# Kernel tuning notes

Measured on AMD Instinct MI355X. Metric: run time of the kernel, lower is better.

Reference implementation:

```python
import jax, jax.numpy as jnp
import numpy as np

D_MODEL, D_HID, N_EXPERTS, TOP_K = 1024, 4096, 8, 2

def setup_inputs() -> dict:
    key = jax.random.key(0)
    ks = jax.random.split(key, 6)
    B, T = 2, 2048
    x = jax.random.normal(ks[0], (B, T, D_MODEL), dtype=jnp.float32)
    gate_w = jax.random.normal(ks[1], (N_EXPERTS, D_MODEL), dtype=jnp.float32) * (1.0 / np.sqrt(D_MODEL))
    # kaiming_uniform-ish init for expert weights
    lim1 = np.sqrt(6.0 / D_MODEL)
    lim2 = np.sqrt(6.0 / D_HID)
    w1 = jax.random.uniform(ks[2], (N_EXPERTS, D_MODEL, D_HID), dtype=jnp.float32, minval=-lim1, maxval=lim1)
    w2 = jax.random.uniform(ks[3], (N_EXPERTS, D_HID, D_MODEL), dtype=jnp.float32, minval=-lim2, maxval=lim2)
    b1 = jnp.zeros((N_EXPERTS, 1, D_HID), dtype=jnp.float32)
    b2 = jnp.zeros((N_EXPERTS, 1, D_MODEL), dtype=jnp.float32)
    return {"x": x, "gate_w": gate_w, "w1": w1, "b1": b1, "w2": w2, "b2": b2}

def reference(x, gate_w, w1, b1, w2, b2):
    B, T, D = x.shape
    E = gate_w.shape[0]
    xf = x.reshape(-1, D)                              # [N, D]
    N = xf.shape[0]
    # Router: logits -> softmax -> top-k -> renormalize
    logits = jnp.einsum('nd,ed->ne', xf, gate_w)       # [N, E]
    scores = jax.nn.softmax(logits, axis=-1)
    top_w, top_i = jax.lax.top_k(scores, TOP_K)        # [N, K]
    top_w = top_w / jnp.sum(top_w, axis=-1, keepdims=True)
    # Dense combine weights (zero for unselected experts) — same math as
    # the padded-bmm dispatch/combine: padded slots have weight 0.
    gates = jnp.zeros((N, E), xf.dtype).at[jnp.arange(N)[:, None], top_i].add(top_w)  # [N, E]
    # Grouped expert MLP (computed densely; weighted combine zeroes unrouted experts)
    h = jax.nn.gelu(jnp.einsum('nd,edh->enh', xf, w1) + b1, approximate=False)  # [E, N, H]
    expert_out = jnp.einsum('enh,ehd->end', h, w2) + b2                          # [E, N, D]
    out = jnp.einsum('end,ne->nd', expert_out, gates)                            # [N, D]
    return out.reshape(B, T, D)
```

## Files before the change

kernel.cpp:

```cpp
#include <hip/hip_runtime.h>
#include <math.h>

#define NTOK 4096
#define DM   1024
#define DH   4096
#define NE   8
#define NSLOT (NTOK*2)
#define TMAX 72

typedef unsigned short u16;
typedef __attribute__((ext_vector_type(8))) short shortx8;
typedef __attribute__((ext_vector_type(4))) float floatx4;
typedef __attribute__((ext_vector_type(4))) int   intx4;

__device__ __forceinline__ u16 f2bf(float f) {
  union { float f; unsigned u; } c; c.f = f;
  unsigned r = c.u + 0x7fffu + ((c.u >> 16) & 1u);
  return (u16)(r >> 16);
}

__device__ __forceinline__ void async_cp16(const u16* g, u16* l) {
  __builtin_amdgcn_global_load_lds(
      (const __attribute__((address_space(1))) void*)g,
      (__attribute__((address_space(3))) void*)l, 16, 0, 0);
}

__global__ void cvt_x_kernel(const float* __restrict__ x, u16* __restrict__ xb) {
  int i = (blockIdx.x * 256 + threadIdx.x) * 8;
  float4 v0 = *(const float4*)(x + i);
  float4 v1 = *(const float4*)(x + i + 4);
  u16 tmp[8] = {f2bf(v0.x), f2bf(v0.y), f2bf(v0.z), f2bf(v0.w),
                f2bf(v1.x), f2bf(v1.y), f2bf(v1.z), f2bf(v1.w)};
  *(intx4*)(xb + i) = *(intx4*)tmp;
}

template<int K, int NW>
__global__ __launch_bounds__(256) void transpose_kernel(const float* __restrict__ W,
                                                        u16* __restrict__ Wt) {
  __shared__ u16 tile[64][66];
  int e = blockIdx.z;
  int n0 = blockIdx.x * 64, k0 = blockIdx.y * 64;
  int tt = threadIdx.x;
  const float* src = W + (size_t)e * K * NW + (size_t)(k0 + (tt >> 2)) * NW + n0 + (tt & 3) * 16;
  int r = tt >> 2, c4 = (tt & 3) * 16;
  float4 v[4];
#pragma unroll
  for (int i = 0; i < 4; i++) v[i] = *(const float4*)(src + i * 4);
#pragma unroll
  for (int i = 0; i < 4; i++) {
    tile[r][c4 + 4 * i + 0] = f2bf(v[i].x);
    tile[r][c4 + 4 * i + 1] = f2bf(v[i].y);
    tile[r][c4 + 4 * i + 2] = f2bf(v[i].z);
    tile[r][c4 + 4 * i + 3] = f2bf(v[i].w);
  }
  __syncthreads();
  u16* dst = Wt + (size_t)e * NW * K + (size_t)n0 * K + k0;
#pragma unroll
  for (int p = 0; p < 2; p++) {
    int n = (tt >> 3) + p * 32;
    int kc = (tt & 7) * 8;
    u16 o[8];
#pragma unroll
    for (int i = 0; i < 8; i++) o[i] = tile[kc + i][n];
    *(intx4*)(dst + (size_t)n * K + kc) = *(intx4*)o;
  }
}

__global__ __launch_bounds__(256) void router_kernel(const float* __restrict__ x,
                                                     const float* __restrict__ gw,
                                                     int* __restrict__ eos,
                                                     float* __restrict__ wos) {
  int wave = threadIdx.x >> 6, lane = threadIdx.x & 63;
  int n = blockIdx.x * 4 + wave;
  const float* xr = x + (size_t)n * DM;
  float acc[NE];
#pragma unroll
  for (int e = 0; e < NE; e++) acc[e] = 0.f;
  for (int d = lane; d < DM; d += 64) {
    float xv = xr[d];
#pragma unroll
    for (int e = 0; e < NE; e++) acc[e] += xv * gw[e * DM + d];
  }
#pragma unroll
  for (int e = 0; e < NE; e++) {
    float v = acc[e];
#pragma unroll
    for (int off = 32; off > 0; off >>= 1) v += __shfl_xor(v, off, 64);
    acc[e] = v;
  }
  if (lane == 0) {
    int i0 = 0;
    for (int e = 1; e < NE; e++) if (acc[e] > acc[i0]) i0 = e;
    int i1 = (i0 == 0) ? 1 : 0;
    for (int e = 0; e < NE; e++) { if (e == i0) continue; if (acc[e] > acc[i1]) i1 = e; }
    float e1 = expf(acc[i1] - acc[i0]);
    float w0 = 1.f / (1.f + e1);
    eos[2 * n] = i0;  eos[2 * n + 1] = i1;
    wos[2 * n] = w0;  wos[2 * n + 1] = 1.f - w0;
  }
}

__global__ __launch_bounds__(256) void build_groups_kernel(
    const int* __restrict__ eos, const float* __restrict__ wos,
    int* __restrict__ goff, int* __restrict__ tok_of_g, float* __restrict__ w_of_g,
    int* __restrict__ tiles, int* __restrict__ ntiles) {
  __shared__ int pref[256][NE];
  __shared__ int tot[NE];
  __shared__ int ebase[NE + 1];
  int t = threadIdx.x;
  int c[NE];
#pragma unroll
  for (int e = 0; e < NE; e++) c[e] = 0;
  for (int i = 0; i < NSLOT / 256; i++) {
    int e = eos[t * (NSLOT / 256) + i];
#pragma unroll
    for (int q = 0; q < NE; q++) if (e == q) c[q]++;
  }
#pragma unroll
  for (int e = 0; e < NE; e++) pref[t][e] = c[e];
  __syncthreads();
  if (t < NE) {
    int run = 0;
    for (int i = 0; i < 256; i++) { int v = pref[i][t]; pref[i][t] = run; run += v; }
    tot[t] = run;
  }
  __syncthreads();
  if (t == 0) {
    int o = 0;
    for (int e = 0; e < NE; e++) { ebase[e] = o; o += tot[e]; }
    ebase[NE] = o;
    int nt = 0;
    for (int e = 0; e < NE; e++)
      for (int mb = 0; mb * 128 < tot[e]; mb++) tiles[nt++] = (e << 16) | mb;
    ntiles[0] = nt;
  }
  __syncthreads();
  int off[NE];
#pragma unroll
  for (int e = 0; e < NE; e++) off[e] = ebase[e] + pref[t][e];
  for (int i = 0; i < NSLOT / 256; i++) {
    int s = t * (NSLOT / 256) + i;
    int e = eos[s];
    int g = 0;
#pragma unroll
    for (int q = 0; q < NE; q++) if (e == q) { g = off[q]; off[q] = g + 1; }
    tok_of_g[g] = s >> 1;
    w_of_g[g] = wos[s];
  }
  if (t <= NE) goff[t] = ebase[t];
}

template<int K, int NOUT, int MODE, int KSPLIT>
__global__ __launch_bounds__(256) void moe_gemm(
    const u16* __restrict__ A, const u16* __restrict__ Wt, const float* __restrict__ bias,
    const int* __restrict__ goff, const int* __restrict__ tok_of_g,
    const float* __restrict__ w_of_g, const int* __restrict__ tiles,
    const int* __restrict__ ntiles,
    u16* __restrict__ Hout, float* __restrict__ Out) {
  const int KLEN = K / KSPLIT;
  int tl = blockIdx.x;
  if (tl >= ntiles[0]) return;
  int packed = tiles[tl];
  int e = packed >> 16;
  int mb = packed & 0xffff;
  int kseg = (KSPLIT > 1) ? blockIdx.z : 0;
  int gb = goff[e];
  int cntE = goff[e + 1] - gb;
  int m0 = mb * 128;
  int mvalid = cntE - m0; if (mvalid > 128) mvalid = 128;
  int gbase = gb + m0;
  int n0 = blockIdx.y * 128;
  int kbeg = kseg * KLEN;
  int tid = threadIdx.x;
  int lane = tid & 63, wave = tid >> 6;

  __shared__ __align__(16) u16 As[128 * 32];
  __shared__ __align__(16) u16 Bs[128 * 32];

  int sr = lane >> 2;
  int sc = (lane & 3) * 8;
  int ra0 = wave * 16 + sr;
  int ra1 = 64 + wave * 16 + sr;
  int ca0 = (ra0 < mvalid) ? ra0 : (mvalid - 1);
  int ca1 = (ra1 < mvalid) ? ra1 : (mvalid - 1);
  const u16 *pa0, *pa1;
  if (MODE == 0) {
    pa0 = A + (size_t)tok_of_g[gbase + ca0] * K + sc;
    pa1 = A + (size_t)tok_of_g[gbase + ca1] * K + sc;
  } else {
    pa0 = A + (size_t)(gbase + ca0) * K + sc;
    pa1 = A + (size_t)(gbase + ca1) * K + sc;
  }
  const u16* wte = Wt + (size_t)e * NOUT * K;
  const u16* pb0 = wte + (size_t)(n0 + ra0) * K + sc;
  const u16* pb1 = wte + (size_t)(n0 + ra1) * K + sc;
  u16* ldsA0 = As + wave * 512;
  u16* ldsA1 = As + 2048 + wave * 512;
  u16* ldsB0 = Bs + wave * 512;
  u16* ldsB1 = Bs + 2048 + wave * 512;

  int wm = wave >> 1, wn = wave & 1;
  int lr = lane & 15, lk = (lane >> 4) * 8;

  floatx4 acc[4][4];
#pragma unroll
  for (int i = 0; i < 4; i++)
#pragma unroll
    for (int j = 0; j < 4; j++) acc[i][j] = (floatx4){0.f, 0.f, 0.f, 0.f};

  for (int k0 = kbeg; k0 < kbeg + KLEN; k0 += 32) {
    __syncthreads();
    async_cp16(pa0 + k0, ldsA0);
    async_cp16(pa1 + k0, ldsA1);
    async_cp16(pb0 + k0, ldsB0);
    async_cp16(pb1 + k0, ldsB1);
    __syncthreads();
    shortx8 af[4], bfr[4];
#pragma unroll
    for (int i = 0; i < 4; i++) {
      af[i]  = *(const shortx8*)&As[(wm * 64 + i * 16 + lr) * 32 + lk];
      bfr[i] = *(const shortx8*)&Bs[(wn * 64 + i * 16 + lr) * 32 + lk];
    }
#pragma unroll
    for (int i = 0; i < 4; i++)
#pragma unroll
      for (int j = 0; j < 4; j++)
        acc[i][j] = __builtin_amdgcn_mfma_f32_16x16x32_bf16(af[i], bfr[j], acc[i][j], 0, 0, 0);
  }

  const float* bp = bias + (size_t)e * NOUT + n0;
  if (MODE == 0) {
#pragma unroll
    for (int i = 0; i < 4; i++) {
      int rowb = wm * 64 + i * 16 + (lane >> 4) * 4;
#pragma unroll
      for (int r = 0; r < 4; r++) {
        int grow = rowb + r;
        if (grow < mvalid) {
          size_t base = (size_t)(gbase + grow) * NOUT + n0;
#pragma unroll
          for (int j = 0; j < 4; j++) {
            int col = wn * 64 + j * 16 + lr;
            float v = acc[i][j][r] + bp[col];
            v = 0.5f * v * (1.f + erff(v * 0.70710678118654752f));
            Hout[base + col] = f2bf(v);
          }
        }
      }
    }
  } else {
#pragma unroll
    for (int i = 0; i < 4; i++) {
      int rowb = wm * 64 + i * 16 + (lane >> 4) * 4;
#pragma unroll
      for (int r = 0; r < 4; r++) {
        int grow = rowb + r;
        if (grow < mvalid) {
          int gi = gbase + grow;
          int t = tok_of_g[gi];
          float wg = w_of_g[gi];
          float* orow = Out + (size_t)t * DM + n0;
#pragma unroll
          for (int j = 0; j < 4; j++) {
            int col = wn * 64 + j * 16 + lr;
            float bb = (kseg == 0) ? bp[col] : 0.f;
            atomicAdd(&orow[col], wg * (acc[i][j][r] + bb));
          }
        }
      }
    }
  }
}

extern "C" void kernel_launch(void* const* d_in, const int* in_sizes, int n_in,
                              void* d_out, int out_size, void* d_ws, size_t ws_size,
                              hipStream_t stream) {
  const float* x  = (const float*)d_in[0];
  const float* gw = (const float*)d_in[1];
  const float* w1 = (const float*)d_in[2];
  const float* b1 = (const float*)d_in[3];
  const float* w2 = (const float*)d_in[4];
  const float* b2 = (const float*)d_in[5];
  float* out = (float*)d_out;
  char* ws = (char*)d_ws;

  u16* xb = (u16*)(ws + 0);
  u16* wt = (u16*)(ws + 8388608);
  u16* h  = (u16*)(ws + 75497472);
  char* meta = ws + 142606336;
  int*   eos      = (int*)(meta);
  int*   tok_of_g = (int*)(meta + 32768);
  float* wos      = (float*)(meta + 65536);
  float* w_of_g   = (float*)(meta + 98304);
  int*   goff     = (int*)(meta + 131072);
  int*   tiles    = (int*)(meta + 131200);
  int*   ntiles   = (int*)(meta + 131584);

  hipMemsetAsync(out, 0, (size_t)NTOK * DM * 4, stream);

  cvt_x_kernel<<<NTOK * DM / 8 / 256, 256, 0, stream>>>(x, xb);
  transpose_kernel<DM, DH><<<dim3(DH / 64, DM / 64, NE), 256, 0, stream>>>(w1, wt);
  router_kernel<<<NTOK / 4, 256, 0, stream>>>(x, gw, eos, wos);
  build_groups_kernel<<<1, 256, 0, stream>>>(eos, wos, goff, tok_of_g, w_of_g, tiles, ntiles);
  moe_gemm<DM, DH, 0, 1><<<dim3(TMAX, DH / 128, 1), 256, 0, stream>>>(
      xb, wt, b1, goff, tok_of_g, w_of_g, tiles, ntiles, h, nullptr);
  transpose_kernel<DH, DM><<<dim3(DM / 64, DH / 64, NE), 256, 0, stream>>>(w2, wt);
  moe_gemm<DH, DM, 1, 2><<<dim3(TMAX, DM / 128, 2), 256, 0, stream>>>(
      h, wt, b2, goff, tok_of_g, w_of_g, tiles, ntiles, nullptr, out);
}
```

Before: 682.4 us.

## Double-buffer LDS tiles in grouped expert GEMM and XOR-swizzle LDS layout

Splits the A and B shared-memory tiles into two buffers so the async global-to-LDS copy of the next K step overlaps the MFMA work on the current one, cutting one barrier per step. It also XOR-swizzles the column offset by row, both on the global source address and on the LDS read index, to reduce LDS bank conflicts on the fragment loads. This doubles the LDS footprint and assumes the K-step count is even and at least 2; correctness relies on the async copy completing by the following barrier.

```diff
diff --git a/kernel.cpp b/kernel.cpp
--- a/kernel.cpp
+++ b/kernel.cpp
@@ -174,33 +174,31 @@
   int tid = threadIdx.x;
   int lane = tid & 63, wave = tid >> 6;
 
-  __shared__ __align__(16) u16 As[128 * 32];
-  __shared__ __align__(16) u16 Bs[128 * 32];
+  __shared__ __align__(16) u16 As[2][128 * 32];
+  __shared__ __align__(16) u16 Bs[2][128 * 32];
 
   int sr = lane >> 2;
   int sc = (lane & 3) * 8;
+  int scs = sc ^ (((sr >> 1) & 3) << 3);
   int ra0 = wave * 16 + sr;
   int ra1 = 64 + wave * 16 + sr;
   int ca0 = (ra0 < mvalid) ? ra0 : (mvalid - 1);
   int ca1 = (ra1 < mvalid) ? ra1 : (mvalid - 1);
   const u16 *pa0, *pa1;
   if (MODE == 0) {
-    pa0 = A + (size_t)tok_of_g[gbase + ca0] * K + sc;
-    pa1 = A + (size_t)tok_of_g[gbase + ca1] * K + sc;
+    pa0 = A + (size_t)tok_of_g[gbase + ca0] * K + scs;
+    pa1 = A + (size_t)tok_of_g[gbase + ca1] * K + scs;
   } else {
-    pa0 = A + (size_t)(gbase + ca0) * K + sc;
-    pa1 = A + (size_t)(gbase + ca1) * K + sc;
+    pa0 = A + (size_t)(gbase + ca0) * K + scs;
+    pa1 = A + (size_t)(gbase + ca1) * K + scs;
   }
   const u16* wte = Wt + (size_t)e * NOUT * K;
-  const u16* pb0 = wte + (size_t)(n0 + ra0) * K + sc;
-  const u16* pb1 = wte + (size_t)(n0 + ra1) * K + sc;
-  u16* ldsA0 = As + wave * 512;
-  u16* ldsA1 = As + 2048 + wave * 512;
-  u16* ldsB0 = Bs + wave * 512;
-  u16* ldsB1 = Bs + 2048 + wave * 512;
+  const u16* pb0 = wte + (size_t)(n0 + ra0) * K + scs;
+  const u16* pb1 = wte + (size_t)(n0 + ra1) * K + scs;
 
   int wm = wave >> 1, wn = wave & 1;
   int lr = lane & 15, lk = (lane >> 4) * 8;
+  int lks = lk ^ (((lr >> 1) & 3) << 3);
 
   floatx4 acc[4][4];
 #pragma unroll
@@ -208,25 +206,41 @@
 #pragma unroll
     for (int j = 0; j < 4; j++) acc[i][j] = (floatx4){0.f, 0.f, 0.f, 0.f};
 
-  for (int k0 = kbeg; k0 < kbeg + KLEN; k0 += 32) {
-    __syncthreads();
-    async_cp16(pa0 + k0, ldsA0);
-    async_cp16(pa1 + k0, ldsA1);
-    async_cp16(pb0 + k0, ldsB0);
-    async_cp16(pb1 + k0, ldsB1);
-    __syncthreads();
+  auto stage = [&](int b, int k0) {
+    async_cp16(pa0 + k0, &As[b][wave * 512]);
+    async_cp16(pa1 + k0, &As[b][2048 + wave * 512]);
+    async_cp16(pb0 + k0, &Bs[b][wave * 512]);
+    async_cp16(pb1 + k0, &Bs[b][2048 + wave * 512]);
+  };
+  auto compute = [&](int b) {
     shortx8 af[4], bfr[4];
 #pragma unroll
     for (int i = 0; i < 4; i++) {
-      af[i]  = *(const shortx8*)&As[(wm * 64 + i * 16 + lr) * 32 + lk];
-      bfr[i] = *(const shortx8*)&Bs[(wn * 64 + i * 16 + lr) * 32 + lk];
+      af[i]  = *(const shortx8*)&As[b][(wm * 64 + i * 16 + lr) * 32 + lks];
+      bfr[i] = *(const shortx8*)&Bs[b][(wn * 64 + i * 16 + lr) * 32 + lks];
     }
 #pragma unroll
     for (int i = 0; i < 4; i++)
 #pragma unroll
       for (int j = 0; j < 4; j++)
         acc[i][j] = __builtin_amdgcn_mfma_f32_16x16x32_bf16(af[i], bfr[j], acc[i][j], 0, 0, 0);
-  }
+  };
+
+  const int NT = KLEN / 32;
+  stage(0, kbeg);
+  __syncthreads();
+  for (int t = 0; t < NT - 2; t += 2) {
+    stage(1, kbeg + (t + 1) * 32);
+    compute(0);
+    __syncthreads();
+    stage(0, kbeg + (t + 2) * 32);
+    compute(1);
+    __syncthreads();
+  }
+  stage(1, kbeg + KLEN - 32);
+  compute(0);
+  __syncthreads();
+  compute(1);
 
   const float* bp = bias + (size_t)e * NOUT + n0;
   if (MODE == 0) {
```

Result: slower. 801.1 us (+17.4%).

## Swizzle LDS layout, remap workgroups XCD-aware with 4x4 super-tiles, raise occupancy hint

Applied to the files above, without the earlier changes.

Three changes to the grouped GEMM. The 2D/3D grid becomes a 1D grid whose block index is remapped so consecutive workgroups on each XCD (flat&7 spread) land in 4x4 super-tiles of (m-tile, n-tile), which improves L2 reuse of A and weight tiles. The LDS layout is XOR-swizzled on the global source column so fragment reads avoid bank conflicts. Launch bounds now request 4 blocks per SM, which may force register limits and cause spills.

```diff
diff --git a/kernel.cpp b/kernel.cpp
--- a/kernel.cpp
+++ b/kernel.cpp
@@ -151,25 +151,33 @@
 }
 
 template<int K, int NOUT, int MODE, int KSPLIT>
-__global__ __launch_bounds__(256) void moe_gemm(
+__global__ __launch_bounds__(256, 4) void moe_gemm(
     const u16* __restrict__ A, const u16* __restrict__ Wt, const float* __restrict__ bias,
     const int* __restrict__ goff, const int* __restrict__ tok_of_g,
     const float* __restrict__ w_of_g, const int* __restrict__ tiles,
     const int* __restrict__ ntiles,
     u16* __restrict__ Hout, float* __restrict__ Out) {
   const int KLEN = K / KSPLIT;
-  int tl = blockIdx.x;
+  const int NB = NOUT / 128;
+  const int NBG = NB / 4;
+  const int NWG = TMAX * NB * KSPLIT;
+  int flat = blockIdx.x;
+  int wgid = (flat & 7) * (NWG >> 3) + (flat >> 3);
+  int kseg = (KSPLIT > 1) ? (wgid / (TMAX * NB)) : 0;
+  int r0w  = wgid % (TMAX * NB);
+  int st = r0w >> 4, within = r0w & 15;
+  int tl = (st / NBG) * 4 + (within >> 2);
+  int nb = (st % NBG) * 4 + (within & 3);
   if (tl >= ntiles[0]) return;
   int packed = tiles[tl];
   int e = packed >> 16;
   int mb = packed & 0xffff;
-  int kseg = (KSPLIT > 1) ? blockIdx.z : 0;
   int gb = goff[e];
   int cntE = goff[e + 1] - gb;
   int m0 = mb * 128;
   int mvalid = cntE - m0; if (mvalid > 128) mvalid = 128;
   int gbase = gb + m0;
-  int n0 = blockIdx.y * 128;
+  int n0 = nb * 128;
   int kbeg = kseg * KLEN;
   int tid = threadIdx.x;
   int lane = tid & 63, wave = tid >> 6;
@@ -179,21 +187,22 @@
 
   int sr = lane >> 2;
   int sc = (lane & 3) * 8;
+  int scs = sc ^ (((sr >> 1) & 3) << 3);
   int ra0 = wave * 16 + sr;
   int ra1 = 64 + wave * 16 + sr;
   int ca0 = (ra0 < mvalid) ? ra0 : (mvalid - 1);
   int ca1 = (ra1 < mvalid) ? ra1 : (mvalid - 1);
   const u16 *pa0, *pa1;
   if (MODE == 0) {
-    pa0 = A + (size_t)tok_of_g[gbase + ca0] * K + sc;
-    pa1 = A + (size_t)tok_of_g[gbase + ca1] * K + sc;
+    pa0 = A + (size_t)tok_of_g[gbase + ca0] * K + scs;
+    pa1 = A + (size_t)tok_of_g[gbase + ca1] * K + scs;
   } else {
-    pa0 = A + (size_t)(gbase + ca0) * K + sc;
-    pa1 = A + (size_t)(gbase + ca1) * K + sc;
+    pa0 = A + (size_t)(gbase + ca0) * K + scs;
+    pa1 = A + (size_t)(gbase + ca1) * K + scs;
   }
   const u16* wte = Wt + (size_t)e * NOUT * K;
-  const u16* pb0 = wte + (size_t)(n0 + ra0) * K + sc;
-  const u16* pb1 = wte + (size_t)(n0 + ra1) * K + sc;
+  const u16* pb0 = wte + (size_t)(n0 + ra0) * K + scs;
+  const u16* pb1 = wte + (size_t)(n0 + ra1) * K + scs;
   u16* ldsA0 = As + wave * 512;
   u16* ldsA1 = As + 2048 + wave * 512;
   u16* ldsB0 = Bs + wave * 512;
@@ -201,6 +210,7 @@
 
   int wm = wave >> 1, wn = wave & 1;
   int lr = lane & 15, lk = (lane >> 4) * 8;
+  int lks = lk ^ (((lr >> 1) & 3) << 3);
 
   floatx4 acc[4][4];
 #pragma unroll
@@ -218,8 +228,8 @@
     shortx8 af[4], bfr[4];
 #pragma unroll
     for (int i = 0; i < 4; i++) {
-      af[i]  = *(const shortx8*)&As[(wm * 64 + i * 16 + lr) * 32 + lk];
-      bfr[i] = *(const shortx8*)&Bs[(wn * 64 + i * 16 + lr) * 32 + lk];
+      af[i]  = *(const shortx8*)&As[(wm * 64 + i * 16 + lr) * 32 + lks];
+      bfr[i] = *(const shortx8*)&Bs[(wn * 64 + i * 16 + lr) * 32 + lks];
     }
 #pragma unroll
     for (int i = 0; i < 4; i++)
@@ -302,9 +312,9 @@
   transpose_kernel<DM, DH><<<dim3(DH / 64, DM / 64, NE), 256, 0, stream>>>(w1, wt);
   router_kernel<<<NTOK / 4, 256, 0, stream>>>(x, gw, eos, wos);
   build_groups_kernel<<<1, 256, 0, stream>>>(eos, wos, goff, tok_of_g, w_of_g, tiles, ntiles);
-  moe_gemm<DM, DH, 0, 1><<<dim3(TMAX, DH / 128, 1), 256, 0, stream>>>(
+  moe_gemm<DM, DH, 0, 1><<<TMAX * (DH / 128), 256, 0, stream>>>(
       xb, wt, b1, goff, tok_of_g, w_of_g, tiles, ntiles, h, nullptr);
   transpose_kernel<DH, DM><<<dim3(DM / 64, DH / 64, NE), 256, 0, stream>>>(w2, wt);
-  moe_gemm<DH, DM, 1, 2><<<dim3(TMAX, DM / 128, 2), 256, 0, stream>>>(
+  moe_gemm<DH, DM, 1, 2><<<TMAX * (DM / 128) * 2, 256, 0, stream>>>(
       h, wt, b2, goff, tok_of_g, w_of_g, tiles, ntiles, nullptr, out);
 }
```

Result: faster. 655.5 us (-3.9%).
